# Kernel optimization log

Hardware: AMD Instinct MI355X
Metric: run time of the kernel (lower is better)

Reference implementation:

```python
import jax, jax.numpy as jnp
import numpy as np

EMB = 512
HEADS = 8
HEAD_DIM = EMB // HEADS


def setup_inputs() -> dict:
    key = jax.random.key(0)
    ks = jax.random.split(key, 9)
    s = 1.0 / np.sqrt(EMB)
    return {
        "x": jax.random.normal(ks[0], (4, 2048, EMB), dtype=jnp.float32),
        "Wq": jax.random.uniform(ks[1], (EMB, EMB), jnp.float32, -s, s),
        "bq": jax.random.uniform(ks[2], (EMB,), jnp.float32, -s, s),
        "Wk": jax.random.uniform(ks[3], (EMB, EMB), jnp.float32, -s, s),
        "bk": jax.random.uniform(ks[4], (EMB,), jnp.float32, -s, s),
        "Wv": jax.random.uniform(ks[5], (EMB, EMB), jnp.float32, -s, s),
        "bv": jax.random.uniform(ks[6], (EMB,), jnp.float32, -s, s),
        "Wp": jax.random.uniform(ks[7], (EMB, EMB), jnp.float32, -s, s),
        "bp": jax.random.uniform(ks[8], (EMB,), jnp.float32, -s, s),
    }


def _split_heads(t):
    b, n, _ = t.shape
    return t.reshape(b, n, HEADS, HEAD_DIM).transpose(0, 2, 1, 3)  # b h n d


def reference(x, Wq, bq, Wk, bk, Wv, bv, Wp, bp):
    q = _split_heads(x @ Wq.T + bq)
    k = _split_heads(x @ Wk.T + bk)
    v = _split_heads(x @ Wv.T + bv)
    energy = jnp.einsum("bhqd,bhkd->bhqk", q, k)
    # NOTE: original applies softmax to UNSCALED logits, then divides probs by sqrt(emb)
    att = jax.nn.softmax(energy, axis=-1) / jnp.sqrt(jnp.float32(EMB))
    out = jnp.einsum("bhqk,bhkd->bhqd", att, v)
    b, h, n, d = out.shape
    out = out.transpose(0, 2, 1, 3).reshape(b, n, h * d)
    return out @ Wp.T + bp
```

## Files before the change

### kernel.cpp

```cpp
#include <hip/hip_runtime.h>
#include <math.h>
#include <stdint.h>

#define SEQ  2048
#define NH   8
#define HD   64
#define MTOT 8192
#define LOG2E 1.4426950408889634f

typedef __attribute__((ext_vector_type(4))) float f32x4;
typedef __attribute__((ext_vector_type(16))) float f32x16;
typedef __attribute__((ext_vector_type(8))) short bf16x8;

template <int V> struct IC { static constexpr int value = V; };

__device__ __forceinline__ unsigned packbf(float a, float b) {
    return __builtin_amdgcn_perm(__float_as_uint(b) + 0x8000u,
                                 __float_as_uint(a) + 0x8000u, 0x07060302u);
}

__global__ __launch_bounds__(256, 3) void qkv_kernel(
    const float* __restrict__ xf, const float* __restrict__ wqf,
    const float* __restrict__ wkf, const float* __restrict__ wvf,
    const float* __restrict__ bq, const float* __restrict__ bk,
    const float* __restrict__ bv,
    unsigned short* __restrict__ Qw, unsigned short* __restrict__ Kw,
    unsigned short* __restrict__ VTw)
{
    __shared__ __align__(16) unsigned short smem[8192];
    unsigned short* As = smem;
    unsigned short* Bs = smem + 4096;

    const int t = threadIdx.x;
    const int w = t >> 6, lane = t & 63, quad = (t >> 4) & 3, l15 = t & 15;
    const int wr = w >> 1, wc = w & 1;
    const int m0 = blockIdx.y * 128;
    const int n0 = blockIdx.x * 128;
    const int which = n0 >> 9;
    const float* wbase = which == 0 ? wqf : (which == 1 ? wkf : wvf);
    const int nrow = n0 & 511;

    const int ar = t >> 2, akq = t & 3;
    const float* ax = xf + (size_t)(m0 + ar) * 512 + akq * 8;
    const float* bx = wbase + (size_t)(nrow + ar) * 512 + akq * 8;
    const int lws = (ar & 15) | (akq << 4);
    const int off0 = (ar >> 4) * 512 + lws * 8;
    const int off1 = off0 + 4 * 512;

    f32x4 acc[4][4];
#pragma unroll
    for (int mt = 0; mt < 4; ++mt)
#pragma unroll
        for (int nt = 0; nt < 4; ++nt) acc[mt][nt] = (f32x4){0.f, 0.f, 0.f, 0.f};

    float4 ra[4], rb[4];
    auto loadt = [&](int k0) {
        ra[0] = *(const float4*)(ax + k0);
        ra[1] = *(const float4*)(ax + k0 + 4);
        ra[2] = *(const float4*)(ax + 32768 + k0);
        ra[3] = *(const float4*)(ax + 32768 + k0 + 4);
        rb[0] = *(const float4*)(bx + k0);
        rb[1] = *(const float4*)(bx + k0 + 4);
        rb[2] = *(const float4*)(bx + 32768 + k0);
        rb[3] = *(const float4*)(bx + 32768 + k0 + 4);
    };
    auto writet = [&]() {
        uint4 p;
        p.x = packbf(ra[0].x, ra[0].y); p.y = packbf(ra[0].z, ra[0].w);
        p.z = packbf(ra[1].x, ra[1].y); p.w = packbf(ra[1].z, ra[1].w);
        *(uint4*)(As + off0) = p;
        p.x = packbf(ra[2].x, ra[2].y); p.y = packbf(ra[2].z, ra[2].w);
        p.z = packbf(ra[3].x, ra[3].y); p.w = packbf(ra[3].z, ra[3].w);
        *(uint4*)(As + off1) = p;
        p.x = packbf(rb[0].x, rb[0].y); p.y = packbf(rb[0].z, rb[0].w);
        p.z = packbf(rb[1].x, rb[1].y); p.w = packbf(rb[1].z, rb[1].w);
        *(uint4*)(Bs + off0) = p;
        p.x = packbf(rb[2].x, rb[2].y); p.y = packbf(rb[2].z, rb[2].w);
        p.z = packbf(rb[3].x, rb[3].y); p.w = packbf(rb[3].z, rb[3].w);
        *(uint4*)(Bs + off1) = p;
    };

    loadt(0);
    auto kloop = [&](auto TRC) {
        constexpr int TR = decltype(TRC)::value;
        for (int ki = 0; ki < 16; ++ki) {
            writet();
            if (ki < 15) loadt((ki + 1) * 32);
            __syncthreads();
            bf16x8 af[4], bfr[4];
#pragma unroll
            for (int mt = 0; mt < 4; ++mt)
                af[mt] = *(const bf16x8*)(As + ((wr * 4 + mt) * 64 + lane) * 8);
#pragma unroll
            for (int nt = 0; nt < 4; ++nt)
                bfr[nt] = *(const bf16x8*)(Bs + ((wc * 4 + nt) * 64 + lane) * 8);
#pragma unroll
            for (int mt = 0; mt < 4; ++mt)
#pragma unroll
                for (int nt = 0; nt < 4; ++nt) {
                    if (TR)
                        acc[mt][nt] = __builtin_amdgcn_mfma_f32_16x16x32_bf16(
                            bfr[nt], af[mt], acc[mt][nt], 0, 0, 0);
                    else
                        acc[mt][nt] = __builtin_amdgcn_mfma_f32_16x16x32_bf16(
                            af[mt], bfr[nt], acc[mt][nt], 0, 0, 0);
                }
            if (ki < 15) __syncthreads();
        }
    };
    if (which < 2) kloop(IC<1>{});
    else           kloop(IC<0>{});

    if (which == 2) {
#pragma unroll
        for (int nt = 0; nt < 4; ++nt) {
            const int n = n0 + wc * 64 + nt * 16 + l15;
            const float bias = bv[n & 511];
            const int h = (n >> 6) & 7, d = n & 63;
#pragma unroll
            for (int mt = 0; mt < 4; ++mt) {
                const int mb = m0 + wr * 64 + mt * 16 + quad * 4;
                const int bi = mb >> 11, ns = mb & 2047;
                const int bhl = bi * 8 + h;
                const f32x4 v = acc[mt][nt];
                uint2 pk;
                pk.x = packbf(v[0] + bias, v[1] + bias);
                pk.y = packbf(v[2] + bias, v[3] + bias);
                const size_t off =
                    ((size_t)(bhl * 32 + (ns >> 6)) * 8 + ((d >> 5) << 2) +
                     ((ns >> 4) & 3)) * 512 +
                    ((d & 31) << 3) + ((ns & 8) << 5) + (ns & 7);
                *(uint2*)(VTw + off) = pk;
            }
        }
    } else {
        const float sc = which ? 1.f : LOG2E;
        const float* bp = which ? bk : bq;
        unsigned short* base = which ? Kw : Qw;
#pragma unroll
        for (int nt = 0; nt < 4; ++nt) {
            const int nb = n0 + wc * 64 + nt * 16 + quad * 4;
            const f32x4 bvv = *(const f32x4*)(bp + (nb & 511));
            const int h = (nb >> 6) & 7, d0 = nb & 63;
#pragma unroll
            for (int mt = 0; mt < 4; ++mt) {
                const int nsg = m0 + wr * 64 + mt * 16 + l15;
                const int bi = nsg >> 11, ns = nsg & 2047;
                const int bhl = bi * 8 + h;
                const f32x4 v = acc[mt][nt];
                uint2 pk;
                pk.x = packbf((v[0] + bvv[0]) * sc, (v[1] + bvv[1]) * sc);
                pk.y = packbf((v[2] + bvv[2]) * sc, (v[3] + bvv[3]) * sc);
                const size_t off =
                    ((size_t)(bhl * 64 + (ns >> 5)) * 4 + (d0 >> 4)) * 512 +
                    ((d0 & 8) << 5) + ((ns & 31) << 3) + (d0 & 7);
                *(uint2*)(base + off) = pk;
            }
        }
    }
}

__global__ __launch_bounds__(256, 3) void outproj_kernel(
    const unsigned short* __restrict__ Aw, const float* __restrict__ wpf,
    const float* __restrict__ bp, float* __restrict__ out)
{
    __shared__ __align__(16) unsigned short smem[6144];
    unsigned short* As = smem;
    unsigned short* Bs = smem + 4096;

    const int t = threadIdx.x;
    const int w = t >> 6, lane = t & 63, quad = (t >> 4) & 3, l15 = t & 15;
    const int wr = w >> 1, wc = w & 1;
    const int m0 = blockIdx.y * 128;
    const int n0 = blockIdx.x * 64;

    const int ar = t >> 2, akq = t & 3;
    const unsigned short* ap = Aw + (size_t)(m0 + ar) * 512 + akq * 8;
    const float* bx = wpf + (size_t)(n0 + ar) * 512 + akq * 8;
    const int lws = (ar & 15) | (akq << 4);
    const int off0 = (ar >> 4) * 512 + lws * 8;
    const int off1 = off0 + 4 * 512;
    const int boff = (ar >> 4) * 512 + lws * 8;

    f32x4 acc[4][2];
#pragma unroll
    for (int mt = 0; mt < 4; ++mt)
#pragma unroll
        for (int nt = 0; nt < 2; ++nt) acc[mt][nt] = (f32x4){0.f, 0.f, 0.f, 0.f};

    uint4 ra0, ra1;
    float4 rb0, rb1;
    auto loadt = [&](int k0) {
        ra0 = *(const uint4*)(ap + k0);
        ra1 = *(const uint4*)(ap + 32768 + k0);
        rb0 = *(const float4*)(bx + k0);
        rb1 = *(const float4*)(bx + k0 + 4);
    };
    auto writet = [&]() {
        *(uint4*)(As + off0) = ra0;
        *(uint4*)(As + off1) = ra1;
        uint4 p;
        p.x = packbf(rb0.x, rb0.y); p.y = packbf(rb0.z, rb0.w);
        p.z = packbf(rb1.x, rb1.y); p.w = packbf(rb1.z, rb1.w);
        *(uint4*)(Bs + boff) = p;
    };

    loadt(0);
    for (int ki = 0; ki < 16; ++ki) {
        writet();
        if (ki < 15) loadt((ki + 1) * 32);
        __syncthreads();
        bf16x8 af[4], bfr[2];
#pragma unroll
        for (int mt = 0; mt < 4; ++mt)
            af[mt] = *(const bf16x8*)(As + ((wr * 4 + mt) * 64 + lane) * 8);
#pragma unroll
        for (int nt = 0; nt < 2; ++nt)
            bfr[nt] = *(const bf16x8*)(Bs + ((wc * 2 + nt) * 64 + lane) * 8);
#pragma unroll
        for (int mt = 0; mt < 4; ++mt)
#pragma unroll
            for (int nt = 0; nt < 2; ++nt)
                acc[mt][nt] = __builtin_amdgcn_mfma_f32_16x16x32_bf16(
                    af[mt], bfr[nt], acc[mt][nt], 0, 0, 0);
        if (ki < 15) __syncthreads();
    }

#pragma unroll
    for (int nt = 0; nt < 2; ++nt) {
        const int n = n0 + wc * 32 + nt * 16 + l15;
        const float bias = bp[n];
#pragma unroll
        for (int mt = 0; mt < 4; ++mt) {
            const int mb = m0 + wr * 64 + mt * 16 + quad * 4;
            const f32x4 v = acc[mt][nt];
#pragma unroll
            for (int r = 0; r < 4; ++r)
                out[(size_t)(mb + r) * 512 + n] = v[r] + bias;
        }
    }
}

__global__ __launch_bounds__(256, 4) void attn_kernel(
    const unsigned short* __restrict__ Qf, const unsigned short* __restrict__ Kf,
    const unsigned short* __restrict__ Vf, unsigned short* __restrict__ Ow)
{
    __shared__ float cb[4224];
    const int t = threadIdx.x;
    const int w = t >> 6, lane = t & 63;
    const int l31 = lane & 31, hlf = lane >> 5;
    const int qh = w >> 1, jh = w & 1;

    const int bh = blockIdx.x;
    const int q0 = blockIdx.y * 64;
    const int qg = (q0 >> 5) + qh;

    const unsigned short* Qp = Qf + ((size_t)(bh * 64 + qg) * 4) * 512 + lane * 8;
    const unsigned short* Kp = Kf + (size_t)bh * 131072 + (jh * 4) * 512 + lane * 8;
    const unsigned short* Vp = Vf + (size_t)bh * 131072 + lane * 8;

    bf16x8 qf[4];
#pragma unroll
    for (int kt = 0; kt < 4; ++kt)
        qf[kt] = *(const bf16x8*)(Qp + kt * 512);

    f32x16 zero;
#pragma unroll
    for (int r = 0; r < 16; ++r) zero[r] = 0.f;

    float lpart = 0.f;
    f32x16 Ot[2];
    Ot[0] = zero; Ot[1] = zero;

    bf16x8 kc[4];
#pragma unroll
    for (int c = 0; c < 4; ++c)
        kc[c] = *(const bf16x8*)(Kp + c * 512);

    for (int jt = 0; jt < 32; ++jt) {
        bf16x8 vc[4];
#pragma unroll
        for (int dg = 0; dg < 2; ++dg)
#pragma unroll
            for (int p = 0; p < 2; ++p)
                vc[dg * 2 + p] = *(const bf16x8*)(
                    Vp + (size_t)jt * 4096 + (dg * 4 + jh * 2 + p) * 512);

        f32x16 st = zero;
#pragma unroll
        for (int kt = 0; kt < 4; ++kt)
            st = __builtin_amdgcn_mfma_f32_32x32x16_bf16(kc[kt], qf[kt], st, 0, 0, 0);

        const int jn = (jt < 31) ? jt + 1 : 31;
#pragma unroll
        for (int c = 0; c < 4; ++c)
            kc[c] = *(const bf16x8*)(Kp + (size_t)jn * 4096 + c * 512);

        float ls = 0.f;
#pragma unroll
        for (int r = 0; r < 16; ++r) {
            st[r] = __builtin_amdgcn_exp2f(st[r]);
            ls += st[r];
        }
        lpart += ls;

        bf16x8 pf[2];
#pragma unroll
        for (int p = 0; p < 2; ++p) {
            const int r0 = p * 8;
            const unsigned a0 = packbf(st[r0 + 0], st[r0 + 1]);
            const unsigned a1 = packbf(st[r0 + 2], st[r0 + 3]);
            const unsigned b0 = packbf(st[r0 + 4], st[r0 + 5]);
            const unsigned b1 = packbf(st[r0 + 6], st[r0 + 7]);
            const unsigned ta0 = (unsigned)__shfl_xor((int)a0, 32);
            const unsigned ta1 = (unsigned)__shfl_xor((int)a1, 32);
            const unsigned tb0 = (unsigned)__shfl_xor((int)b0, 32);
            const unsigned tb1 = (unsigned)__shfl_xor((int)b1, 32);
            union { unsigned u[4]; bf16x8 v; } pb;
            pb.u[0] = hlf ? tb0 : a0;
            pb.u[1] = hlf ? tb1 : a1;
            pb.u[2] = hlf ? b0 : ta0;
            pb.u[3] = hlf ? b1 : ta1;
            pf[p] = pb.v;
        }

#pragma unroll
        for (int dg = 0; dg < 2; ++dg)
#pragma unroll
            for (int p = 0; p < 2; ++p)
                Ot[dg] = __builtin_amdgcn_mfma_f32_32x32x16_bf16(
                    vc[dg * 2 + p], pf[p], Ot[dg], 0, 0, 0);
    }

    if (jh == 1) {
#pragma unroll
        for (int dg = 0; dg < 2; ++dg)
#pragma unroll
            for (int k = 0; k < 4; ++k) {
                float4 v = make_float4(Ot[dg][k * 4 + 0], Ot[dg][k * 4 + 1],
                                       Ot[dg][k * 4 + 2], Ot[dg][k * 4 + 3]);
                *(float4*)(cb + ((qh * 2 + dg) * 4 + k) * 256 + lane * 4) = v;
            }
        cb[4096 + qh * 64 + lane] = lpart;
    }
    __syncthreads();
    if (jh == 0) {
#pragma unroll
        for (int dg = 0; dg < 2; ++dg)
#pragma unroll
            for (int k = 0; k < 4; ++k) {
                const float4 v =
                    *(const float4*)(cb + ((qh * 2 + dg) * 4 + k) * 256 + lane * 4);
                Ot[dg][k * 4 + 0] += v.x; Ot[dg][k * 4 + 1] += v.y;
                Ot[dg][k * 4 + 2] += v.z; Ot[dg][k * 4 + 3] += v.w;
            }
        float lv = lpart + cb[4096 + qh * 64 + lane];
        lv += __shfl_xor(lv, 32);
        const float inv = 1.0f / (lv * 22.627416997969522f);

        const int bi = bh >> 3, h = bh & 7;
        const int ns = q0 + qh * 32 + l31;
        unsigned short* dst = Ow + ((size_t)bi * SEQ + ns) * 512 + h * 64 + hlf * 4;
#pragma unroll
        for (int dg = 0; dg < 2; ++dg)
#pragma unroll
            for (int rb = 0; rb < 4; ++rb) {
                uint2 pk;
                pk.x = packbf(Ot[dg][rb * 4 + 0] * inv, Ot[dg][rb * 4 + 1] * inv);
                pk.y = packbf(Ot[dg][rb * 4 + 2] * inv, Ot[dg][rb * 4 + 3] * inv);
                *(uint2*)(dst + dg * 32 + rb * 8) = pk;
            }
    }
}

extern "C" void kernel_launch(void* const* d_in, const int* in_sizes, int n_in,
                              void* d_out, int out_size, void* d_ws, size_t ws_size,
                              hipStream_t stream)
{
    const float* x  = (const float*)d_in[0];
    const float* Wq = (const float*)d_in[1];
    const float* bq = (const float*)d_in[2];
    const float* Wk = (const float*)d_in[3];
    const float* bk = (const float*)d_in[4];
    const float* Wv = (const float*)d_in[5];
    const float* bv = (const float*)d_in[6];
    const float* Wp = (const float*)d_in[7];
    const float* bp = (const float*)d_in[8];

    unsigned short* ws = (unsigned short*)d_ws;
    unsigned short* Qw  = ws;
    unsigned short* Kw  = Qw + 4194304;
    unsigned short* VTw = Kw + 4194304;
    unsigned short* Owb = VTw + 4194304;

    qkv_kernel<<<dim3(12, 64), 256, 0, stream>>>(
        x, Wq, Wk, Wv, bq, bk, bv, Qw, Kw, VTw);
    attn_kernel<<<dim3(32, 32), 256, 0, stream>>>(Qw, Kw, VTw, Owb);
    outproj_kernel<<<dim3(8, 64), 256, 0, stream>>>(Owb, Wp, bp, (float*)d_out);
}
```

Measured before the change: 169.6 us.

## Process two query tiles per warp in attention to reuse K/V fragments

Each attention warp now computes two 32-row query groups instead of one, so every loaded K and V fragment feeds twice as many MFMAs. The block covers 128 queries, the grid's y dimension is halved, and the shared combine buffer doubles. In exchange, register pressure rises (launch bounds lowered to 2 blocks per SIMD-level target) and there are fewer blocks, which could reduce occupancy and latency hiding. The row-sum reduction is also rewritten as a pairwise tree.

```diff
diff --git a/kernel.cpp b/kernel.cpp
--- a/kernel.cpp
+++ b/kernel.cpp
@@ -3,9 +3,6 @@
 #include <stdint.h>
 
 #define SEQ  2048
-#define NH   8
-#define HD   64
-#define MTOT 8192
 #define LOG2E 1.4426950408889634f
 
 typedef __attribute__((ext_vector_type(4))) float f32x4;
@@ -135,12 +132,12 @@
         }
     } else {
         const float sc = which ? 1.f : LOG2E;
-        const float* bp = which ? bk : bq;
+        const float* bpt = which ? bk : bq;
         unsigned short* base = which ? Kw : Qw;
 #pragma unroll
         for (int nt = 0; nt < 4; ++nt) {
             const int nb = n0 + wc * 64 + nt * 16 + quad * 4;
-            const f32x4 bvv = *(const f32x4*)(bp + (nb & 511));
+            const f32x4 bvv = *(const f32x4*)(bpt + (nb & 511));
             const int h = (nb >> 6) & 7, d0 = nb & 63;
 #pragma unroll
             for (int mt = 0; mt < 4; ++mt) {
@@ -241,36 +238,40 @@
     }
 }
 
-__global__ __launch_bounds__(256, 4) void attn_kernel(
+__global__ __launch_bounds__(256, 2) void attn_kernel(
     const unsigned short* __restrict__ Qf, const unsigned short* __restrict__ Kf,
     const unsigned short* __restrict__ Vf, unsigned short* __restrict__ Ow)
 {
-    __shared__ float cb[4224];
+    __shared__ float cb[8448];
     const int t = threadIdx.x;
     const int w = t >> 6, lane = t & 63;
     const int l31 = lane & 31, hlf = lane >> 5;
     const int qh = w >> 1, jh = w & 1;
 
     const int bh = blockIdx.x;
-    const int q0 = blockIdx.y * 64;
-    const int qg = (q0 >> 5) + qh;
-
-    const unsigned short* Qp = Qf + ((size_t)(bh * 64 + qg) * 4) * 512 + lane * 8;
+    const int qblk = blockIdx.y;
+    const int q0 = qblk * 128;
+
     const unsigned short* Kp = Kf + (size_t)bh * 131072 + (jh * 4) * 512 + lane * 8;
     const unsigned short* Vp = Vf + (size_t)bh * 131072 + lane * 8;
 
-    bf16x8 qf[4];
-#pragma unroll
-    for (int kt = 0; kt < 4; ++kt)
-        qf[kt] = *(const bf16x8*)(Qp + kt * 512);
+    bf16x8 qf[2][4];
+#pragma unroll
+    for (int qg = 0; qg < 2; ++qg) {
+        const int qgg = qblk * 4 + qh * 2 + qg;
+        const unsigned short* Qp = Qf + ((size_t)(bh * 64 + qgg) * 4) * 512 + lane * 8;
+#pragma unroll
+        for (int kt = 0; kt < 4; ++kt)
+            qf[qg][kt] = *(const bf16x8*)(Qp + kt * 512);
+    }
 
     f32x16 zero;
 #pragma unroll
     for (int r = 0; r < 16; ++r) zero[r] = 0.f;
 
-    float lpart = 0.f;
-    f32x16 Ot[2];
-    Ot[0] = zero; Ot[1] = zero;
+    float lpart[2] = {0.f, 0.f};
+    f32x16 Ot[2][2];
+    Ot[0][0] = zero; Ot[0][1] = zero; Ot[1][0] = zero; Ot[1][1] = zero;
 
     bf16x8 kc[4];
 #pragma unroll
@@ -286,90 +287,116 @@
                 vc[dg * 2 + p] = *(const bf16x8*)(
                     Vp + (size_t)jt * 4096 + (dg * 4 + jh * 2 + p) * 512);
 
-        f32x16 st = zero;
-#pragma unroll
-        for (int kt = 0; kt < 4; ++kt)
-            st = __builtin_amdgcn_mfma_f32_32x32x16_bf16(kc[kt], qf[kt], st, 0, 0, 0);
+        f32x16 st[2];
+        st[0] = zero; st[1] = zero;
+#pragma unroll
+        for (int kt = 0; kt < 4; ++kt) {
+            st[0] = __builtin_amdgcn_mfma_f32_32x32x16_bf16(kc[kt], qf[0][kt], st[0], 0, 0, 0);
+            st[1] = __builtin_amdgcn_mfma_f32_32x32x16_bf16(kc[kt], qf[1][kt], st[1], 0, 0, 0);
+        }
 
         const int jn = (jt < 31) ? jt + 1 : 31;
 #pragma unroll
         for (int c = 0; c < 4; ++c)
             kc[c] = *(const bf16x8*)(Kp + (size_t)jn * 4096 + c * 512);
 
-        float ls = 0.f;
-#pragma unroll
-        for (int r = 0; r < 16; ++r) {
-            st[r] = __builtin_amdgcn_exp2f(st[r]);
-            ls += st[r];
-        }
-        lpart += ls;
-
-        bf16x8 pf[2];
-#pragma unroll
-        for (int p = 0; p < 2; ++p) {
-            const int r0 = p * 8;
-            const unsigned a0 = packbf(st[r0 + 0], st[r0 + 1]);
-            const unsigned a1 = packbf(st[r0 + 2], st[r0 + 3]);
-            const unsigned b0 = packbf(st[r0 + 4], st[r0 + 5]);
-            const unsigned b1 = packbf(st[r0 + 6], st[r0 + 7]);
-            const unsigned ta0 = (unsigned)__shfl_xor((int)a0, 32);
-            const unsigned ta1 = (unsigned)__shfl_xor((int)a1, 32);
-            const unsigned tb0 = (unsigned)__shfl_xor((int)b0, 32);
-            const unsigned tb1 = (unsigned)__shfl_xor((int)b1, 32);
-            union { unsigned u[4]; bf16x8 v; } pb;
-            pb.u[0] = hlf ? tb0 : a0;
-            pb.u[1] = hlf ? tb1 : a1;
-            pb.u[2] = hlf ? b0 : ta0;
-            pb.u[3] = hlf ? b1 : ta1;
-            pf[p] = pb.v;
-        }
+#pragma unroll
+        for (int qg = 0; qg < 2; ++qg) {
+#pragma unroll
+            for (int r = 0; r < 16; ++r)
+                st[qg][r] = __builtin_amdgcn_exp2f(st[qg][r]);
+            float s01 = st[qg][0] + st[qg][1],   s23 = st[qg][2] + st[qg][3];
+            float s45 = st[qg][4] + st[qg][5],   s67 = st[qg][6] + st[qg][7];
+            float s89 = st[qg][8] + st[qg][9],   sAB = st[qg][10] + st[qg][11];
+            float sCD = st[qg][12] + st[qg][13], sEF = st[qg][14] + st[qg][15];
+            lpart[qg] += ((s01 + s23) + (s45 + s67)) + ((s89 + sAB) + (sCD + sEF));
+        }
+
+        bf16x8 pf[2][2];
+#pragma unroll
+        for (int qg = 0; qg < 2; ++qg)
+#pragma unroll
+            for (int p = 0; p < 2; ++p) {
+                const int r0 = p * 8;
+                const unsigned a0 = packbf(st[qg][r0 + 0], st[qg][r0 + 1]);
+                const unsigned a1 = packbf(st[qg][r0 + 2], st[qg][r0 + 3]);
+                const unsigned b0 = packbf(st[qg][r0 + 4], st[qg][r0 + 5]);
+                const unsigned b1 = packbf(st[qg][r0 + 6], st[qg][r0 + 7]);
+                const unsigned ta0 = (unsigned)__shfl_xor((int)a0, 32);
+                const unsigned ta1 = (unsigned)__shfl_xor((int)a1, 32);
+                const unsigned tb0 = (unsigned)__shfl_xor((int)b0, 32);
+                const unsigned tb1 = (unsigned)__shfl_xor((int)b1, 32);
+                union { unsigned u[4]; bf16x8 v; } pb;
+                pb.u[0] = hlf ? tb0 : a0;
+                pb.u[1] = hlf ? tb1 : a1;
+                pb.u[2] = hlf ? b0 : ta0;
+                pb.u[3] = hlf ? b1 : ta1;
+                pf[qg][p] = pb.v;
+            }
 
 #pragma unroll
         for (int dg = 0; dg < 2; ++dg)
 #pragma unroll
-            for (int p = 0; p < 2; ++p)
-                Ot[dg] = __builtin_amdgcn_mfma_f32_32x32x16_bf16(
-                    vc[dg * 2 + p], pf[p], Ot[dg], 0, 0, 0);
+            for (int p = 0; p < 2; ++p) {
+                Ot[0][dg] = __builtin_amdgcn_mfma_f32_32x32x16_bf16(
+                    vc[dg * 2 + p], pf[0][p], Ot[0][dg], 0, 0, 0);
+                Ot[1][dg] = __builtin_amdgcn_mfma_f32_32x32x16_bf16(
+                    vc[dg * 2 + p], pf[1][p], Ot[1][dg], 0, 0, 0);
+            }
     }
 
     if (jh == 1) {
 #pragma unroll
-        for (int dg = 0; dg < 2; ++dg)
-#pragma unroll
-            for (int k = 0; k < 4; ++k) {
-                float4 v = make_float4(Ot[dg][k * 4 + 0], Ot[dg][k * 4 + 1],
-                                       Ot[dg][k * 4 + 2], Ot[dg][k * 4 + 3]);
-                *(float4*)(cb + ((qh * 2 + dg) * 4 + k) * 256 + lane * 4) = v;
-            }
-        cb[4096 + qh * 64 + lane] = lpart;
+        for (int qg = 0; qg < 2; ++qg) {
+#pragma unroll
+            for (int dg = 0; dg < 2; ++dg) {
+                const int cidx = ((qh * 2 + qg) * 2 + dg) * 4;
+#pragma unroll
+                for (int k = 0; k < 4; ++k) {
+                    float4 v = make_float4(
+                        Ot[qg][dg][k * 4 + 0], Ot[qg][dg][k * 4 + 1],
+                        Ot[qg][dg][k * 4 + 2], Ot[qg][dg][k * 4 + 3]);
+                    *(float4*)(cb + (cidx + k) * 256 + lane * 4) = v;
+                }
+            }
+            cb[8192 + (qh * 2 + qg) * 64 + lane] = lpart[qg];
+        }
     }
     __syncthreads();
     if (jh == 0) {
-#pragma unroll
-        for (int dg = 0; dg < 2; ++dg)
-#pragma unroll
-            for (int k = 0; k < 4; ++k) {
-                const float4 v =
-                    *(const float4*)(cb + ((qh * 2 + dg) * 4 + k) * 256 + lane * 4);
-                Ot[dg][k * 4 + 0] += v.x; Ot[dg][k * 4 + 1] += v.y;
-                Ot[dg][k * 4 + 2] += v.z; Ot[dg][k * 4 + 3] += v.w;
-            }
-        float lv = lpart + cb[4096 + qh * 64 + lane];
-        lv += __shfl_xor(lv, 32);
-        const float inv = 1.0f / (lv * 22.627416997969522f);
-
         const int bi = bh >> 3, h = bh & 7;
-        const int ns = q0 + qh * 32 + l31;
-        unsigned short* dst = Ow + ((size_t)bi * SEQ + ns) * 512 + h * 64 + hlf * 4;
-#pragma unroll
-        for (int dg = 0; dg < 2; ++dg)
-#pragma unroll
-            for (int rb = 0; rb < 4; ++rb) {
-                uint2 pk;
-                pk.x = packbf(Ot[dg][rb * 4 + 0] * inv, Ot[dg][rb * 4 + 1] * inv);
-                pk.y = packbf(Ot[dg][rb * 4 + 2] * inv, Ot[dg][rb * 4 + 3] * inv);
-                *(uint2*)(dst + dg * 32 + rb * 8) = pk;
-            }
+#pragma unroll
+        for (int qg = 0; qg < 2; ++qg) {
+#pragma unroll
+            for (int dg = 0; dg < 2; ++dg) {
+                const int cidx = ((qh * 2 + qg) * 2 + dg) * 4;
+#pragma unroll
+                for (int k = 0; k < 4; ++k) {
+                    const float4 v = *(const float4*)(cb + (cidx + k) * 256 + lane * 4);
+                    Ot[qg][dg][k * 4 + 0] += v.x;
+                    Ot[qg][dg][k * 4 + 1] += v.y;
+                    Ot[qg][dg][k * 4 + 2] += v.z;
+                    Ot[qg][dg][k * 4 + 3] += v.w;
+                }
+            }
+            float lv = lpart[qg] + cb[8192 + (qh * 2 + qg) * 64 + lane];
+            lv += __shfl_xor(lv, 32);
+            const float inv = 1.0f / (lv * 22.627416997969522f);
+
+            const int ns = q0 + (qh * 2 + qg) * 32 + l31;
+            unsigned short* dst = Ow + ((size_t)bi * SEQ + ns) * 512 + h * 64 + hlf * 4;
+#pragma unroll
+            for (int dg = 0; dg < 2; ++dg)
+#pragma unroll
+                for (int rb2 = 0; rb2 < 4; ++rb2) {
+                    uint2 pk;
+                    pk.x = packbf(Ot[qg][dg][rb2 * 4 + 0] * inv,
+                                  Ot[qg][dg][rb2 * 4 + 1] * inv);
+                    pk.y = packbf(Ot[qg][dg][rb2 * 4 + 2] * inv,
+                                  Ot[qg][dg][rb2 * 4 + 3] * inv);
+                    *(uint2*)(dst + dg * 32 + rb2 * 8) = pk;
+                }
+        }
     }
 }
 
@@ -395,6 +422,6 @@
 
     qkv_kernel<<<dim3(12, 64), 256, 0, stream>>>(
         x, Wq, Wk, Wv, bq, bk, bv, Qw, Kw, VTw);
-    attn_kernel<<<dim3(32, 32), 256, 0, stream>>>(Qw, Kw, VTw, Owb);
+    attn_kernel<<<dim3(32, 16), 256, 0, stream>>>(Qw, Kw, VTw, Owb);
     outproj_kernel<<<dim3(8, 64), 256, 0, stream>>>(Owb, Wp, bp, (float*)d_out);
 }
```

Result: no change. 168.9 us (-0.4%).

## Double-buffer GEMM shared tiles and software-pipeline QK^T in attention loop

Applied to the files above, without the earlier changes.

The QKV and output-projection GEMMs now ping-pong between two shared-memory buffers, so each k-step needs one barrier instead of two and the write of the next tile overlaps the current MFMAs. The attention loop computes the next block's QK^T scores one iteration ahead, which lets the exp2 and PV work on the current block overlap with MFMA latency. It also tree-reduces the row sum and unrolls the loop by 2. The cost is doubled LDS per GEMM block, which can lower occupancy, and more live registers in the attention kernel.

```diff
diff --git a/kernel.cpp b/kernel.cpp
--- a/kernel.cpp
+++ b/kernel.cpp
@@ -3,9 +3,6 @@
 #include <stdint.h>
 
 #define SEQ  2048
-#define NH   8
-#define HD   64
-#define MTOT 8192
 #define LOG2E 1.4426950408889634f
 
 typedef __attribute__((ext_vector_type(4))) float f32x4;
@@ -27,9 +24,9 @@
     unsigned short* __restrict__ Qw, unsigned short* __restrict__ Kw,
     unsigned short* __restrict__ VTw)
 {
-    __shared__ __align__(16) unsigned short smem[8192];
+    __shared__ __align__(16) unsigned short smem[16384];
     unsigned short* As = smem;
-    unsigned short* Bs = smem + 4096;
+    unsigned short* Bs = smem + 8192;
 
     const int t = threadIdx.x;
     const int w = t >> 6, lane = t & 63, quad = (t >> 4) & 3, l15 = t & 15;
@@ -64,36 +61,38 @@
         rb[2] = *(const float4*)(bx + 32768 + k0);
         rb[3] = *(const float4*)(bx + 32768 + k0 + 4);
     };
-    auto writet = [&]() {
+    auto writet = [&](int buf) {
+        const int bo = buf * 4096;
         uint4 p;
         p.x = packbf(ra[0].x, ra[0].y); p.y = packbf(ra[0].z, ra[0].w);
         p.z = packbf(ra[1].x, ra[1].y); p.w = packbf(ra[1].z, ra[1].w);
-        *(uint4*)(As + off0) = p;
+        *(uint4*)(As + bo + off0) = p;
         p.x = packbf(ra[2].x, ra[2].y); p.y = packbf(ra[2].z, ra[2].w);
         p.z = packbf(ra[3].x, ra[3].y); p.w = packbf(ra[3].z, ra[3].w);
-        *(uint4*)(As + off1) = p;
+        *(uint4*)(As + bo + off1) = p;
         p.x = packbf(rb[0].x, rb[0].y); p.y = packbf(rb[0].z, rb[0].w);
         p.z = packbf(rb[1].x, rb[1].y); p.w = packbf(rb[1].z, rb[1].w);
-        *(uint4*)(Bs + off0) = p;
+        *(uint4*)(Bs + bo + off0) = p;
         p.x = packbf(rb[2].x, rb[2].y); p.y = packbf(rb[2].z, rb[2].w);
         p.z = packbf(rb[3].x, rb[3].y); p.w = packbf(rb[3].z, rb[3].w);
-        *(uint4*)(Bs + off1) = p;
+        *(uint4*)(Bs + bo + off1) = p;
     };
 
     loadt(0);
+    writet(0);
     auto kloop = [&](auto TRC) {
         constexpr int TR = decltype(TRC)::value;
         for (int ki = 0; ki < 16; ++ki) {
-            writet();
+            __syncthreads();
             if (ki < 15) loadt((ki + 1) * 32);
-            __syncthreads();
+            const int bo = (ki & 1) * 4096;
             bf16x8 af[4], bfr[4];
 #pragma unroll
             for (int mt = 0; mt < 4; ++mt)
-                af[mt] = *(const bf16x8*)(As + ((wr * 4 + mt) * 64 + lane) * 8);
+                af[mt] = *(const bf16x8*)(As + bo + ((wr * 4 + mt) * 64 + lane) * 8);
 #pragma unroll
             for (int nt = 0; nt < 4; ++nt)
-                bfr[nt] = *(const bf16x8*)(Bs + ((wc * 4 + nt) * 64 + lane) * 8);
+                bfr[nt] = *(const bf16x8*)(Bs + bo + ((wc * 4 + nt) * 64 + lane) * 8);
 #pragma unroll
             for (int mt = 0; mt < 4; ++mt)
 #pragma unroll
@@ -105,7 +104,7 @@
                         acc[mt][nt] = __builtin_amdgcn_mfma_f32_16x16x32_bf16(
                             af[mt], bfr[nt], acc[mt][nt], 0, 0, 0);
                 }
-            if (ki < 15) __syncthreads();
+            if (ki < 15) writet((ki + 1) & 1);
         }
     };
     if (which < 2) kloop(IC<1>{});
@@ -135,12 +134,12 @@
         }
     } else {
         const float sc = which ? 1.f : LOG2E;
-        const float* bp = which ? bk : bq;
+        const float* bpt = which ? bk : bq;
         unsigned short* base = which ? Kw : Qw;
 #pragma unroll
         for (int nt = 0; nt < 4; ++nt) {
             const int nb = n0 + wc * 64 + nt * 16 + quad * 4;
-            const f32x4 bvv = *(const f32x4*)(bp + (nb & 511));
+            const f32x4 bvv = *(const f32x4*)(bpt + (nb & 511));
             const int h = (nb >> 6) & 7, d0 = nb & 63;
 #pragma unroll
             for (int mt = 0; mt < 4; ++mt) {
@@ -164,9 +163,9 @@
     const unsigned short* __restrict__ Aw, const float* __restrict__ wpf,
     const float* __restrict__ bp, float* __restrict__ out)
 {
-    __shared__ __align__(16) unsigned short smem[6144];
+    __shared__ __align__(16) unsigned short smem[12288];
     unsigned short* As = smem;
-    unsigned short* Bs = smem + 4096;
+    unsigned short* Bs = smem + 8192;
 
     const int t = threadIdx.x;
     const int w = t >> 6, lane = t & 63, quad = (t >> 4) & 3, l15 = t & 15;
@@ -196,34 +195,35 @@
         rb0 = *(const float4*)(bx + k0);
         rb1 = *(const float4*)(bx + k0 + 4);
     };
-    auto writet = [&]() {
-        *(uint4*)(As + off0) = ra0;
-        *(uint4*)(As + off1) = ra1;
+    auto writet = [&](int buf) {
+        *(uint4*)(As + buf * 4096 + off0) = ra0;
+        *(uint4*)(As + buf * 4096 + off1) = ra1;
         uint4 p;
         p.x = packbf(rb0.x, rb0.y); p.y = packbf(rb0.z, rb0.w);
         p.z = packbf(rb1.x, rb1.y); p.w = packbf(rb1.z, rb1.w);
-        *(uint4*)(Bs + boff) = p;
+        *(uint4*)(Bs + buf * 2048 + boff) = p;
     };
 
     loadt(0);
+    writet(0);
     for (int ki = 0; ki < 16; ++ki) {
-        writet();
+        __syncthreads();
         if (ki < 15) loadt((ki + 1) * 32);
-        __syncthreads();
+        const int ba = (ki & 1) * 4096, bb = (ki & 1) * 2048;
         bf16x8 af[4], bfr[2];
 #pragma unroll
         for (int mt = 0; mt < 4; ++mt)
-            af[mt] = *(const bf16x8*)(As + ((wr * 4 + mt) * 64 + lane) * 8);
+            af[mt] = *(const bf16x8*)(As + ba + ((wr * 4 + mt) * 64 + lane) * 8);
 #pragma unroll
         for (int nt = 0; nt < 2; ++nt)
-            bfr[nt] = *(const bf16x8*)(Bs + ((wc * 2 + nt) * 64 + lane) * 8);
+            bfr[nt] = *(const bf16x8*)(Bs + bb + ((wc * 2 + nt) * 64 + lane) * 8);
 #pragma unroll
         for (int mt = 0; mt < 4; ++mt)
 #pragma unroll
             for (int nt = 0; nt < 2; ++nt)
                 acc[mt][nt] = __builtin_amdgcn_mfma_f32_16x16x32_bf16(
                     af[mt], bfr[nt], acc[mt][nt], 0, 0, 0);
-        if (ki < 15) __syncthreads();
+        if (ki < 15) writet((ki + 1) & 1);
     }
 
 #pragma unroll
@@ -276,8 +276,29 @@
 #pragma unroll
     for (int c = 0; c < 4; ++c)
         kc[c] = *(const bf16x8*)(Kp + c * 512);
-
+    f32x16 st_cur = zero;
+#pragma unroll
+    for (int kt = 0; kt < 4; ++kt)
+        st_cur = __builtin_amdgcn_mfma_f32_32x32x16_bf16(kc[kt], qf[kt], st_cur, 0, 0, 0);
+#pragma unroll
+    for (int c = 0; c < 4; ++c)
+        kc[c] = *(const bf16x8*)(Kp + 4096 + c * 512);
+
+#pragma unroll 2
     for (int jt = 0; jt < 32; ++jt) {
+        f32x16 st_next = zero;
+        if (jt < 31) {
+#pragma unroll
+            for (int kt = 0; kt < 4; ++kt)
+                st_next = __builtin_amdgcn_mfma_f32_32x32x16_bf16(
+                    kc[kt], qf[kt], st_next, 0, 0, 0);
+        }
+        {
+            const int j2 = (jt < 30) ? jt + 2 : 31;
+#pragma unroll
+            for (int c = 0; c < 4; ++c)
+                kc[c] = *(const bf16x8*)(Kp + (size_t)j2 * 4096 + c * 512);
+        }
         bf16x8 vc[4];
 #pragma unroll
         for (int dg = 0; dg < 2; ++dg)
@@ -286,32 +307,25 @@
                 vc[dg * 2 + p] = *(const bf16x8*)(
                     Vp + (size_t)jt * 4096 + (dg * 4 + jh * 2 + p) * 512);
 
-        f32x16 st = zero;
-#pragma unroll
-        for (int kt = 0; kt < 4; ++kt)
-            st = __builtin_amdgcn_mfma_f32_32x32x16_bf16(kc[kt], qf[kt], st, 0, 0, 0);
-
-        const int jn = (jt < 31) ? jt + 1 : 31;
-#pragma unroll
-        for (int c = 0; c < 4; ++c)
-            kc[c] = *(const bf16x8*)(Kp + (size_t)jn * 4096 + c * 512);
-
-        float ls = 0.f;
-#pragma unroll
-        for (int r = 0; r < 16; ++r) {
-            st[r] = __builtin_amdgcn_exp2f(st[r]);
-            ls += st[r];
-        }
-        lpart += ls;
+#pragma unroll
+        for (int r = 0; r < 16; ++r)
+            st_cur[r] = __builtin_amdgcn_exp2f(st_cur[r]);
+        {
+            float s01 = st_cur[0] + st_cur[1],   s23 = st_cur[2] + st_cur[3];
+            float s45 = st_cur[4] + st_cur[5],   s67 = st_cur[6] + st_cur[7];
+            float s89 = st_cur[8] + st_cur[9],   sAB = st_cur[10] + st_cur[11];
+            float sCD = st_cur[12] + st_cur[13], sEF = st_cur[14] + st_cur[15];
+            lpart += ((s01 + s23) + (s45 + s67)) + ((s89 + sAB) + (sCD + sEF));
+        }
 
         bf16x8 pf[2];
 #pragma unroll
         for (int p = 0; p < 2; ++p) {
             const int r0 = p * 8;
-            const unsigned a0 = packbf(st[r0 + 0], st[r0 + 1]);
-            const unsigned a1 = packbf(st[r0 + 2], st[r0 + 3]);
-            const unsigned b0 = packbf(st[r0 + 4], st[r0 + 5]);
-            const unsigned b1 = packbf(st[r0 + 6], st[r0 + 7]);
+            const unsigned a0 = packbf(st_cur[r0 + 0], st_cur[r0 + 1]);
+            const unsigned a1 = packbf(st_cur[r0 + 2], st_cur[r0 + 3]);
+            const unsigned b0 = packbf(st_cur[r0 + 4], st_cur[r0 + 5]);
+            const unsigned b1 = packbf(st_cur[r0 + 6], st_cur[r0 + 7]);
             const unsigned ta0 = (unsigned)__shfl_xor((int)a0, 32);
             const unsigned ta1 = (unsigned)__shfl_xor((int)a1, 32);
             const unsigned tb0 = (unsigned)__shfl_xor((int)b0, 32);
@@ -330,6 +344,8 @@
             for (int p = 0; p < 2; ++p)
                 Ot[dg] = __builtin_amdgcn_mfma_f32_32x32x16_bf16(
                     vc[dg * 2 + p], pf[p], Ot[dg], 0, 0, 0);
+
+        st_cur = st_next;
     }
 
     if (jh == 1) {
```

Result: slower. 192.9 us (+13.7%).
